# Performance work log

Measured on AMD Instinct MI355X. Metric: run time of the kernel, lower is better.

## Reference

```python
import jax, jax.numpy as jnp
import numpy as np

W = 1022      # window_length (fft_length) -> 512 rfft bins
HOP = 256     # hop_length
F = 64        # frames
ORDER = 5     # butterworth order
WN = 0.5      # normalized cutoff (cutoff = fs/4)

# ---- Butterworth lowpass design (scipy.signal.butter equivalent, numpy only) ----
def _butter_lowpass(order, wn):
    m = np.arange(-order + 1, order, 2)
    p = -np.exp(1j * np.pi * m / (2 * order))        # analog prototype poles
    k = 1.0
    fs = 2.0
    warped = 2 * fs * np.tan(np.pi * wn / fs)        # pre-warp
    p = p * warped                                   # lp2lp
    k = k * warped ** order
    fs2 = 2 * fs                                     # bilinear
    pd = (fs2 + p) / (fs2 - p)
    zd = -np.ones(order)
    kd = k * np.real(1.0 / np.prod(fs2 - p))
    b = np.real(kd * np.poly(zd))
    a = np.real(np.poly(pd))
    return b / a[0], a / a[0]

_B_NP, _A_NP = _butter_lowpass(ORDER, WN)

def _lfilter_zi(b, a):
    n = max(len(a), len(b))
    A = np.zeros((n - 1, n - 1))
    A[0, :] = -a[1:]
    A[1:, :-1] = np.eye(n - 2)
    A = A.T
    Bv = b[1:] - a[1:] * b[0]
    return np.linalg.solve(np.eye(n - 1) - A, Bv)

_ZI_NP = _lfilter_zi(_B_NP, _A_NP)
PADLEN = 3 * max(len(_A_NP), len(_B_NP))  # scipy filtfilt default = 18

B_COEF = jnp.asarray(_B_NP, jnp.float32)
A_COEF = jnp.asarray(_A_NP, jnp.float32)
ZI = jnp.asarray(_ZI_NP, jnp.float32)

# ---- windows (tf.signal defaults: periodic Hann; inverse_stft_window_fn) ----
def _hann(n):
    return 0.5 - 0.5 * np.cos(2.0 * np.pi * np.arange(n) / n)

_FW = _hann(W)
_overlaps = -(-W // HOP)
_den = np.pad(_FW ** 2, (0, _overlaps * HOP - W))
_den = _den.reshape(_overlaps, HOP).sum(0)
_den = np.tile(_den, _overlaps)[:W]
SYN_WIN = jnp.asarray(_FW / _den, jnp.float32)   # synthesis window
FWD_WIN = jnp.asarray(_FW, jnp.float32)          # analysis window

_IDX = np.arange(F)[:, None] * HOP + np.arange(W)[None, :]  # [F, W]
T = HOP * (F - 1) + W  # 17150


def _lfilter(x, zi):
    # direct-form II transposed, batched over axis 0; x: [B,T], zi: [B,n]
    b0, b1, a1 = B_COEF[0], B_COEF[1:], A_COEF[1:]
    def step(z, xt):
        y = b0 * xt + z[:, 0]
        zs = jnp.concatenate([z[:, 1:], jnp.zeros_like(z[:, :1])], axis=1)
        z = zs + xt[:, None] * b1[None, :] - y[:, None] * a1[None, :]
        return z, y
    _, ys = jax.lax.scan(step, zi, x.T)
    return ys.T


def _filtfilt(x):
    # scipy.signal.filtfilt with padtype='odd', padlen=PADLEN
    left = 2.0 * x[:, :1] - x[:, PADLEN:0:-1]
    right = 2.0 * x[:, -1:] - x[:, -2:-PADLEN - 2:-1]
    xe = jnp.concatenate([left, x, right], axis=1)
    y = _lfilter(xe, ZI[None, :] * xe[:, :1])
    y = y[:, ::-1]
    y = _lfilter(y, ZI[None, :] * y[:, :1])
    y = y[:, ::-1]
    return y[:, PADLEN:-PADLEN]


def setup_inputs() -> dict:
    key = jax.random.key(0)
    x = jax.random.normal(key, (64, 512, F, 2), dtype=jnp.float32)
    return {"x": x}


def reference(x):
    bsz = x.shape[0]
    stfts = jax.lax.complex(x[..., 0], x[..., 1])          # [B,512,F]
    frames = jnp.transpose(stfts, (0, 2, 1))               # [B,F,512]
    # inverse STFT: irfft -> synthesis window -> overlap-add
    sig_frames = jnp.fft.irfft(frames, n=W, axis=-1) * SYN_WIN  # [B,F,W]
    signals = jnp.zeros((bsz, T), jnp.float32).at[:, _IDX.reshape(-1)].add(
        sig_frames.reshape(bsz, -1))                       # [B,T]
    filt = _filtfilt(signals)                              # [B,T]
    # forward STFT
    fr = filt[:, _IDX] * FWD_WIN                           # [B,F,W]
    S = jnp.fft.rfft(fr, n=W, axis=-1)                     # [B,F,512]
    S = jnp.transpose(S, (0, 2, 1))                        # [B,512,F]
    return jnp.stack([jnp.real(S), jnp.imag(S)], axis=-1)
```

## Files before the change

### kernel.cpp

```cpp
#include <hip/hip_runtime.h>
#include <cmath>
#include <complex>
#include <algorithm>

#define NW      1022
#define NB      64
#define TLEN    17150
#define PADL    18
#define LXLEN   17186
#define NFRAMES 4096
#define GK      1024
#define BS      4288
#define SPAN    4480

typedef __attribute__((ext_vector_type(8))) short short8;
typedef __attribute__((ext_vector_type(4))) float floatx4;

struct IirCoef {
  float b0,b1,b2,b3,b4,b5;
  float a1,a2,a3,a4,a5;
  float zi0,zi1,zi2,zi3,zi4;
};

static __device__ __forceinline__ ushort f2bf(float f) {
  uint32_t u = __builtin_bit_cast(uint32_t, f);
  uint32_t r = (u + 0x7FFFu + ((u >> 16) & 1u)) >> 16;
  return (ushort)r;
}
static __device__ __forceinline__ float bf2f(ushort u) {
  return __builtin_bit_cast(float, (uint32_t)u << 16);
}

static __device__ __forceinline__ float phase_mod(int k, int t) {
  const float TPN = 6.2831853071795864769f / 1022.f;
  float kt = (float)(k * t);
  float q = floorf(kt * (1.0f / 1022.0f));
  float r = kt - q * 1022.0f;
  if (r < 0.f) r += 1022.f;
  if (r >= 1022.f) r -= 1022.f;
  return r * TPN;
}

__global__ __launch_bounds__(256) void prep(const float* __restrict__ x,
                                            ushort* __restrict__ BT1,
                                            ushort* __restrict__ BT2,
                                            ushort* __restrict__ A1) {
  __shared__ float tile[32][129];
  const float TPN = 6.2831853071795864769f / 1022.f;
  int bid = blockIdx.x;
  if (bid < 4096) {
    int idx = bid * 256 + threadIdx.x;
    int t = idx >> 10, kk = idx & 1023;
    int k = kk & 511;
    float val = 0.f;
    if (t < NW) {
      float fw = 0.5f - 0.5f * __cosf((float)t * TPN);
      float den = 0.f;
      int tm = t & 255;
      #pragma unroll
      for (int j = 0; j < 4; ++j) {
        int u = tm + (j << 8);
        if (u < NW) { float w = 0.5f - 0.5f * __cosf((float)u * TPN); den += w * w; }
      }
      float syn = fw / den;
      float arg = phase_mod(k, t);
      float scale = (k == 0 || k == 511) ? 1.f : 2.f;
      if (kk < 512) val = __cosf(arg) * scale * (1.f / 1022.f) * syn;
      else          val = (k == 0 || k == 511) ? 0.f
                          : -__sinf(arg) * scale * (1.f / 1022.f) * syn;
    }
    BT1[idx] = f2bf(val);
  } else if (bid < 8192) {
    int idx = (bid - 4096) * 256 + threadIdx.x;
    int kk = idx >> 10, t = idx & 1023;
    int k = kk & 511;
    float val = 0.f;
    if (t < NW) {
      float fw = 0.5f - 0.5f * __cosf((float)t * TPN);
      float arg = phase_mod(k, t);
      val = (kk < 512) ? fw * __cosf(arg) : -fw * __sinf(arg);
    }
    BT2[idx] = f2bf(val);
  } else {
    int tb = bid - 8192;
    int b  = tb >> 4;
    int k0 = (tb & 15) << 5;
    int tid = threadIdx.x;
    #pragma unroll
    for (int e = 0; e < 16; ++e) {
      int lin = tid + e * 256;
      int i = lin >> 7, c = lin & 127;
      tile[i][c] = x[(b * 512 + k0 + i) * 128 + c];
    }
    __syncthreads();
    #pragma unroll
    for (int e = 0; e < 16; ++e) {
      int lin = tid + e * 256;
      int c = lin >> 5, i = lin & 31;
      int f = c >> 1, ri = c & 1;
      A1[(b * 64 + f) * 1024 + ri * 512 + k0 + i] = f2bf(tile[i][c]);
    }
  }
}

#define GLOAD16(gsrc, ldst) \
  __builtin_amdgcn_global_load_lds( \
      (const __attribute__((address_space(1))) void*)(gsrc), \
      (__attribute__((address_space(3))) void*)(ldst), 16, 0, 0)

#define WAIT_VMCNT6()  __builtin_amdgcn_s_waitcnt(0xF76)
#define WAIT_VMCNT0()  __builtin_amdgcn_s_waitcnt(0xF70)

static __device__ __forceinline__ void gemm_compute64(
    const ushort* as, const ushort* bs, int arow, int brow, int g, int rx,
    floatx4 (&acc)[2][4]) {
  #pragma unroll
  for (int ks = 0; ks < 2; ++ks) {
    short8 af[2], bfr[4];
    const int chunk = ((ks << 2) + g) ^ rx;
    #pragma unroll
    for (int fm = 0; fm < 2; ++fm)
      af[fm] = *(const short8*)(as + (arow + fm * 16) * 64 + chunk * 8);
    #pragma unroll
    for (int fn = 0; fn < 4; ++fn)
      bfr[fn] = *(const short8*)(bs + (brow + fn * 16) * 64 + chunk * 8);
    #pragma unroll
    for (int fm = 0; fm < 2; ++fm)
      #pragma unroll
      for (int fn = 0; fn < 4; ++fn)
        acc[fm][fn] = __builtin_amdgcn_mfma_f32_16x16x32_bf16(
            af[fm], bfr[fn], acc[fm][fn], 0, 0, 0);
  }
}

__global__ __launch_bounds__(256, 3) void gemm1(
    const ushort* __restrict__ A, const ushort* __restrict__ Bt,
    ushort* __restrict__ Fr) {
  __shared__ __align__(16) ushort As[2][64 * 64];
  __shared__ __align__(16) ushort Bs[2][128 * 64];
  const int tid = threadIdx.x;
  const int wid = tid >> 6, lane = tid & 63;
  const int m0 = blockIdx.y * 64, n0 = blockIdx.x * 128;
  const int warp_m = wid >> 1, warp_n = wid & 1;

  floatx4 acc[2][4];
  #pragma unroll
  for (int i = 0; i < 2; ++i)
    #pragma unroll
    for (int j = 0; j < 4; ++j) acc[i][j] = (floatx4){0.f, 0.f, 0.f, 0.f};

  const int lr = lane >> 3, lc = lane & 7;
  const int swz = lc ^ lr;
  const ushort* aBase = A  + (size_t)(m0 + wid * 8 + lr) * GK + swz * 8;
  const ushort* bBase = Bt + (size_t)(n0 + wid * 8 + lr) * GK + swz * 8;

  const int lane15 = lane & 15;
  const int g = lane >> 4;
  const int rx = lane & 7;
  const int arow = warp_m * 32 + lane15;
  const int brow = warp_n * 64 + lane15;

#define STAGE_G1(buf, kk0) do { \
    _Pragma("unroll") \
    for (int p = 0; p < 2; ++p) \
      GLOAD16(aBase + (size_t)(p * 32) * GK + (kk0), &As[buf][(p * 32 + wid * 8) * 64]); \
    _Pragma("unroll") \
    for (int p = 0; p < 4; ++p) \
      GLOAD16(bBase + (size_t)(p * 32) * GK + (kk0), &Bs[buf][(p * 32 + wid * 8) * 64]); \
    } while (0)

  STAGE_G1(0, 0);
  for (int t = 0; t < 15; ++t) {
    STAGE_G1((t + 1) & 1, (t + 1) * 64);
    WAIT_VMCNT6();
    __builtin_amdgcn_s_barrier();
    __builtin_amdgcn_sched_barrier(0);
    gemm_compute64(&As[t & 1][0], &Bs[t & 1][0], arow, brow, g, rx, acc);
    __builtin_amdgcn_sched_barrier(0);
    __builtin_amdgcn_s_barrier();
  }
  WAIT_VMCNT0();
  __builtin_amdgcn_s_barrier();
  gemm_compute64(&As[1][0], &Bs[1][0], arow, brow, g, rx, acc);

  #pragma unroll
  for (int fm = 0; fm < 2; ++fm)
    #pragma unroll
    for (int fn = 0; fn < 4; ++fn)
      #pragma unroll
      for (int i = 0; i < 4; ++i) {
        int gm = m0 + warp_m * 32 + fm * 16 + g * 4 + i;
        int gn = n0 + warp_n * 64 + fn * 16 + lane15;
        Fr[(size_t)gm * 1024 + gn] = f2bf(acc[fm][fn][i]);
      }
#undef STAGE_G1
}

__global__ __launch_bounds__(256, 3) void gemm2(
    const ushort* __restrict__ Ftb, const ushort* __restrict__ Bt,
    float* __restrict__ out) {
  __shared__ __align__(16) ushort smem[2 * 64 * 64 + 2 * 128 * 64];
  ushort (*As)[64 * 64] = (ushort(*)[64 * 64])smem;
  ushort (*Bs)[128 * 64] = (ushort(*)[128 * 64])(smem + 2 * 64 * 64);
  float* CT = (float*)smem;
  const int tid = threadIdx.x;
  const int wid = tid >> 6, lane = tid & 63;
  const int by = blockIdx.y, bx = blockIdx.x;
  const int warp_m = wid >> 1, warp_n = wid & 1;

  floatx4 acc[2][4];
  #pragma unroll
  for (int i = 0; i < 2; ++i)
    #pragma unroll
    for (int j = 0; j < 4; ++j) acc[i][j] = (floatx4){0.f, 0.f, 0.f, 0.f};

  const int lr = lane >> 3, lc = lane & 7;
  const int swz = lc ^ lr;

  const ushort* aBase = Ftb + (size_t)by * TLEN + (wid * 8 + lr) * 256 + swz * 8;
  const ushort* bB0 = Bt + (size_t)(bx * 64 + wid * 8 + lr) * GK + swz * 8;

  const int lane15 = lane & 15;
  const int g = lane >> 4;
  const int rx = lane & 7;
  const int arow = warp_m * 32 + lane15;
  const int brow = warp_n * 64 + lane15;

#define STAGE_G2(buf, kk0) do { \
    _Pragma("unroll") \
    for (int p = 0; p < 2; ++p) \
      GLOAD16(aBase + (size_t)(p * 32) * 256 + (kk0), &As[buf][(p * 32 + wid * 8) * 64]); \
    _Pragma("unroll") \
    for (int p = 0; p < 4; ++p) { \
      size_t boff = (size_t)((p & 1) * 32 + (p >> 1) * 512) * GK; \
      GLOAD16(bB0 + boff + (kk0), &Bs[buf][(((p >> 1) * 64 + (p & 1) * 32) + wid * 8) * 64]); \
    } } while (0)

  STAGE_G2(0, 0);
  for (int t = 0; t < 15; ++t) {
    STAGE_G2((t + 1) & 1, (t + 1) * 64);
    WAIT_VMCNT6();
    __builtin_amdgcn_s_barrier();
    __builtin_amdgcn_sched_barrier(0);
    gemm_compute64(&As[t & 1][0], &Bs[t & 1][0], arow, brow, g, rx, acc);
    __builtin_amdgcn_sched_barrier(0);
    __builtin_amdgcn_s_barrier();
  }
  WAIT_VMCNT0();
  __builtin_amdgcn_s_barrier();
  gemm_compute64(&As[1][0], &Bs[1][0], arow, brow, g, rx, acc);

  __syncthreads();
  #pragma unroll
  for (int fm = 0; fm < 2; ++fm)
    #pragma unroll
    for (int fn = 0; fn < 4; ++fn)
      #pragma unroll
      for (int i = 0; i < 4; ++i) {
        int s    = warp_n * 64 + fn * 16 + lane15;
        int fcol = warp_m * 32 + fm * 16 + g * 4 + i;
        CT[s * 65 + fcol] = acc[fm][fn][i];
      }
  __syncthreads();
  #pragma unroll
  for (int e = 0; e < 8; ++e) {
    int it = tid + e * 256;
    int r = it >> 5, q = it & 31;
    float4 v;
    v.x = CT[r * 65 + 2 * q];
    v.y = CT[(64 + r) * 65 + 2 * q];
    v.z = CT[r * 65 + 2 * q + 1];
    v.w = CT[(64 + r) * 65 + 2 * q + 1];
    *(float4*)&out[((size_t)(by * 512 + bx * 64 + r)) * 128 + q * 4] = v;
  }
#undef STAGE_G2
}

#define SWZ(r) ((r) ^ (((r) >> 6) & 31))

static __device__ __forceinline__ float oa_sample(const ushort* __restrict__ frb,
                                                  int tau) {
  int fhi = tau >> 8;
  int flo = fhi - 3; if (flo < 0) flo = 0;
  if (fhi > 63) fhi = 63;
  float sum = 0.f;
  for (int f = flo; f <= fhi; ++f) {
    int off = tau - (f << 8);
    if (off < NW) sum += bf2f(frb[(size_t)f * 1024 + off]);
  }
  return sum;
}

#define IIR_STEP(x, y)                                   \
  float y = fmaf(cf.b0, (x), z0);                        \
  z0 = fmaf(-cf.a1, y, fmaf(cf.b1, (x), z1));            \
  z1 = fmaf(-cf.a2, y, fmaf(cf.b2, (x), z2));            \
  z2 = fmaf(-cf.a3, y, fmaf(cf.b3, (x), z3));            \
  z3 = fmaf(-cf.a4, y, fmaf(cf.b4, (x), z4));            \
  z4 = fmaf(-cf.a5, y, cf.b5 * (x));

__global__ __launch_bounds__(256) void oa_iir(const ushort* __restrict__ Fr,
                                              ushort* __restrict__ Ftb,
                                              IirCoef cf) {
  __shared__ float bufX[SPAN];
  __shared__ float bufY[SPAN];
  const int blk = blockIdx.x;
  const int b = blk >> 2, sp = blk & 3;
  const int lo = sp * BS;
  const int hi = (lo + BS < TLEN) ? lo + BS : TLEN;
  const int F0 = (sp == 0) ? 0 : lo + PADL;
  int F1 = hi + PADL + 128; if (F1 > LXLEN) F1 = LXLEN;
  const int XB = (sp == 0) ? 0 : F0 - 64;
  const int xspan = F1 - XB;
  const ushort* frb = Fr + (size_t)(b * 64) * 1024;

  for (int rel = threadIdx.x; rel < xspan; rel += 256) {
    int p = XB + rel;
    float v;
    if (p < PADL)
      v = 2.f * oa_sample(frb, 0) - oa_sample(frb, PADL - p);
    else if (p < PADL + TLEN)
      v = oa_sample(frb, p - PADL);
    else {
      int j = p - (PADL + TLEN);
      v = 2.f * oa_sample(frb, TLEN - 1) - oa_sample(frb, TLEN - 2 - j);
    }
    bufX[SWZ(rel)] = v;
  }
  __syncthreads();

  {
    int nch = (F1 - F0 + 63) >> 6;
    int c = threadIdx.x;
    if (c < nch) {
      int os = F0 + (c << 6);
      int oe = os + 64; if (oe > F1) oe = F1;
      float z0, z1, z2, z3, z4;
      int i;
      if (sp == 0 && c == 0) {
        float x0 = bufX[SWZ(0)];
        z0 = cf.zi0 * x0; z1 = cf.zi1 * x0; z2 = cf.zi2 * x0;
        z3 = cf.zi3 * x0; z4 = cf.zi4 * x0;
        i = 0;
      } else {
        z0 = z1 = z2 = z3 = z4 = 0.f;
        i = os - 64;
        #pragma unroll 4
        for (; i < os; ++i) { float x = bufX[SWZ(i - XB)]; IIR_STEP(x, y); (void)y; }
      }
      #pragma unroll 4
      for (; i < oe; ++i) {
        float x = bufX[SWZ(i - XB)];
        IIR_STEP(x, y);
        bufY[SWZ(i - XB)] = y;
      }
    }
  }
  __syncthreads();

  {
    const int R0 = TLEN + PADL - hi;
    const int R1 = LXLEN - lo - PADL;
    int k_lo = R0 >> 6, k_hi = (R1 - 1) >> 6;
    int k = k_lo + threadIdx.x;
    if (k <= k_hi) {
      int rs = k << 6;
      int re = rs + 64; if (re > R1) re = R1;
      float z0, z1, z2, z3, z4;
      int i;
      if (k == 0) {
        float x0 = bufY[SWZ(LXLEN - 1 - XB)];
        z0 = cf.zi0 * x0; z1 = cf.zi1 * x0; z2 = cf.zi2 * x0;
        z3 = cf.zi3 * x0; z4 = cf.zi4 * x0;
        i = 0;
      } else {
        z0 = z1 = z2 = z3 = z4 = 0.f;
        i = rs - 64;
        #pragma unroll 4
        for (; i < rs; ++i) { float x = bufY[SWZ(LXLEN - 1 - i - XB)]; IIR_STEP(x, y); (void)y; }
      }
      #pragma unroll 4
      for (; i < re; ++i) {
        float x = bufY[SWZ(LXLEN - 1 - i - XB)];
        IIR_STEP(x, y);
        if (i >= R0) bufX[SWZ(LXLEN - 1 - i - XB)] = y;
      }
    }
  }
  __syncthreads();

  for (int t = lo + threadIdx.x; t < hi; t += 256)
    Ftb[(size_t)b * TLEN + t] = f2bf(bufX[SWZ(t + PADL - XB)]);
  if (b == NB - 1 && sp == 3)
    for (int t = threadIdx.x; t < 1024; t += 256)
      Ftb[(size_t)NB * TLEN + t] = 0;
}

static void solve5(double M[5][5], double v[5], double outv[5]) {
  for (int col = 0; col < 5; ++col) {
    int piv = col;
    for (int r = col + 1; r < 5; ++r)
      if (std::fabs(M[r][col]) > std::fabs(M[piv][col])) piv = r;
    if (piv != col) {
      for (int c = 0; c < 5; ++c) std::swap(M[col][c], M[piv][c]);
      std::swap(v[col], v[piv]);
    }
    double d = M[col][col];
    for (int r = col + 1; r < 5; ++r) {
      double f = M[r][col] / d;
      for (int c = col; c < 5; ++c) M[r][c] -= f * M[col][c];
      v[r] -= f * v[col];
    }
  }
  for (int r = 4; r >= 0; --r) {
    double s = v[r];
    for (int c = r + 1; c < 5; ++c) s -= M[r][c] * outv[c];
    outv[r] = s / M[r][r];
  }
}

static IirCoef make_coef() {
  const double PI = 3.14159265358979323846;
  std::complex<double> p[5];
  for (int i = 0; i < 5; ++i) {
    double m = -4.0 + 2.0 * i;
    p[i] = -std::exp(std::complex<double>(0.0, PI * m / 10.0));
  }
  double fs = 2.0;
  double warped = 2.0 * fs * std::tan(PI * 0.5 / fs);
  for (int i = 0; i < 5; ++i) p[i] *= warped;
  double kgain = std::pow(warped, 5.0);
  double fs2 = 2.0 * fs;
  std::complex<double> pd[5], prod(1.0, 0.0);
  for (int i = 0; i < 5; ++i) {
    pd[i] = (fs2 + p[i]) / (fs2 - p[i]);
    prod *= (fs2 - p[i]);
  }
  double kd = kgain * std::real(1.0 / prod);
  double b[6] = {kd, 5 * kd, 10 * kd, 10 * kd, 5 * kd, kd};
  std::complex<double> c[6] = {{1,0},{0,0},{0,0},{0,0},{0,0},{0,0}};
  for (int i = 0; i < 5; ++i)
    for (int j = i + 1; j >= 1; --j)
      c[j] -= pd[i] * c[j - 1];
  double a[6]; for (int i = 0; i < 6; ++i) a[i] = c[i].real();
  double M[5][5], v[5];
  for (int r = 0; r < 5; ++r)
    for (int cc = 0; cc < 5; ++cc) {
      double Af = 0.0;
      if (cc == 0) Af = -a[r + 1];
      if (cc == r + 1) Af = 1.0;
      M[r][cc] = (r == cc ? 1.0 : 0.0) - Af;
    }
  for (int r = 0; r < 5; ++r) v[r] = b[r + 1] - a[r + 1] * b[0];
  double zi[5];
  solve5(M, v, zi);
  IirCoef cf;
  cf.b0 = (float)b[0]; cf.b1 = (float)b[1]; cf.b2 = (float)b[2];
  cf.b3 = (float)b[3]; cf.b4 = (float)b[4]; cf.b5 = (float)b[5];
  cf.a1 = (float)a[1]; cf.a2 = (float)a[2]; cf.a3 = (float)a[3];
  cf.a4 = (float)a[4]; cf.a5 = (float)a[5];
  cf.zi0 = (float)zi[0]; cf.zi1 = (float)zi[1]; cf.zi2 = (float)zi[2];
  cf.zi3 = (float)zi[3]; cf.zi4 = (float)zi[4];
  return cf;
}

extern "C" void kernel_launch(void* const* d_in, const int* in_sizes, int n_in,
                              void* d_out, int out_size, void* d_ws, size_t ws_size,
                              hipStream_t stream) {
  const float* x = (const float*)d_in[0];
  float* out = (float*)d_out;

  ushort* BT1 = (ushort*)d_ws;
  ushort* BT2 = BT1 + 1024 * 1024;
  ushort* A1  = BT2 + 1024 * 1024;
  ushort* Ftb = A1 + (size_t)NFRAMES * 1024;
  ushort* Fr  = Ftb + (size_t)NB * TLEN + 1024;
  size_t need = (size_t)((char*)(Fr + (size_t)NFRAMES * 1024) - (char*)d_ws);
  if (ws_size < need) return;

  IirCoef cf = make_coef();

  prep<<<9216, 256, 0, stream>>>(x, BT1, BT2, A1);
  gemm1<<<dim3(8, 64), 256, 0, stream>>>(A1, BT1, Fr);
  oa_iir<<<NB * 4, 256, 0, stream>>>(Fr, Ftb, cf);
  gemm2<<<dim3(8, 64), 256, 0, stream>>>(Ftb, BT2, out);
}
```

Before: 81.75 us.

## Split IIR into 8 spans, vectorize twiddle prep, move BT2 build into gemm1

The IIR/overlap-add kernel now splits each batch row into 8 spans instead of 4, doubling block count from 256 to 512 for better CU occupancy, at the cost of more warm-up recomputation at span boundaries. The BT1 twiddle generation writes 4 bf16 values per thread with a vector store. BT2 generation moves out of prep into extra blocks of gemm1 so it overlaps with the first GEMM. gemm1 also remaps block indices so neighbouring tiles land on the same XCD for L2 locality.

```diff
diff --git a/kernel.cpp b/kernel.cpp
--- a/kernel.cpp
+++ b/kernel.cpp
@@ -10,10 +10,12 @@
 #define LXLEN   17186
 #define NFRAMES 4096
 #define GK      1024
-#define BS      4288
-#define SPAN    4480
+#define NSPLIT  8
+#define BS      2144
+#define SPAN    2336
 
 typedef __attribute__((ext_vector_type(8))) short short8;
+typedef __attribute__((ext_vector_type(4))) short short4v;
 typedef __attribute__((ext_vector_type(4))) float floatx4;
 
 struct IirCoef {
@@ -43,16 +45,14 @@
 
 __global__ __launch_bounds__(256) void prep(const float* __restrict__ x,
                                             ushort* __restrict__ BT1,
-                                            ushort* __restrict__ BT2,
                                             ushort* __restrict__ A1) {
   __shared__ float tile[32][129];
   const float TPN = 6.2831853071795864769f / 1022.f;
   int bid = blockIdx.x;
-  if (bid < 4096) {
-    int idx = bid * 256 + threadIdx.x;
-    int t = idx >> 10, kk = idx & 1023;
-    int k = kk & 511;
-    float val = 0.f;
+  if (bid < 1024) {
+    int idx4 = (bid * 256 + threadIdx.x) * 4;
+    int t = idx4 >> 10, kk0 = idx4 & 1023;
+    short4v v = (short4v){0, 0, 0, 0};
     if (t < NW) {
       float fw = 0.5f - 0.5f * __cosf((float)t * TPN);
       float den = 0.f;
@@ -63,26 +63,21 @@
         if (u < NW) { float w = 0.5f - 0.5f * __cosf((float)u * TPN); den += w * w; }
       }
       float syn = fw / den;
-      float arg = phase_mod(k, t);
-      float scale = (k == 0 || k == 511) ? 1.f : 2.f;
-      if (kk < 512) val = __cosf(arg) * scale * (1.f / 1022.f) * syn;
-      else          val = (k == 0 || k == 511) ? 0.f
-                          : -__sinf(arg) * scale * (1.f / 1022.f) * syn;
-    }
-    BT1[idx] = f2bf(val);
-  } else if (bid < 8192) {
-    int idx = (bid - 4096) * 256 + threadIdx.x;
-    int kk = idx >> 10, t = idx & 1023;
-    int k = kk & 511;
-    float val = 0.f;
-    if (t < NW) {
-      float fw = 0.5f - 0.5f * __cosf((float)t * TPN);
-      float arg = phase_mod(k, t);
-      val = (kk < 512) ? fw * __cosf(arg) : -fw * __sinf(arg);
-    }
-    BT2[idx] = f2bf(val);
+      #pragma unroll
+      for (int e = 0; e < 4; ++e) {
+        int kk = kk0 + e, k = kk & 511;
+        float arg = phase_mod(k, t);
+        float scale = (k == 0 || k == 511) ? 1.f : 2.f;
+        float val;
+        if (kk < 512) val = __cosf(arg) * scale * (1.f / 1022.f) * syn;
+        else          val = (k == 0 || k == 511) ? 0.f
+                            : -__sinf(arg) * scale * (1.f / 1022.f) * syn;
+        v[e] = (short)f2bf(val);
+      }
+    }
+    *(short4v*)&BT1[idx4] = v;
   } else {
-    int tb = bid - 8192;
+    int tb = bid - 1024;
     int b  = tb >> 4;
     int k0 = (tb & 15) << 5;
     int tid = threadIdx.x;
@@ -135,19 +130,46 @@
 
 __global__ __launch_bounds__(256, 3) void gemm1(
     const ushort* __restrict__ A, const ushort* __restrict__ Bt,
-    ushort* __restrict__ Fr) {
+    ushort* __restrict__ Fr, ushort* __restrict__ BT2) {
   __shared__ __align__(16) ushort As[2][64 * 64];
   __shared__ __align__(16) ushort Bs[2][128 * 64];
+  const float TPN = 6.2831853071795864769f / 1022.f;
+
+  if (blockIdx.y >= 64) {
+    int bid = (blockIdx.y - 64) * 8 + blockIdx.x;
+    int idx4 = (bid * 256 + threadIdx.x) * 4;
+    int kk = idx4 >> 10, t0 = idx4 & 1023;
+    int k = kk & 511;
+    short4v v = (short4v){0, 0, 0, 0};
+    #pragma unroll
+    for (int e = 0; e < 4; ++e) {
+      int t = t0 + e;
+      if (t < NW) {
+        float fw = 0.5f - 0.5f * __cosf((float)t * TPN);
+        float arg = phase_mod(k, t);
+        float val = (kk < 512) ? fw * __cosf(arg) : -fw * __sinf(arg);
+        v[e] = (short)f2bf(val);
+      }
+    }
+    *(short4v*)&BT2[idx4] = v;
+    return;
+  }
+
+  const int L = blockIdx.x + 8 * blockIdx.y;
+  const int xcd = L & 7, j = L >> 3;
+  const int by_n = xcd * 8 + (j & 7);
+  const int bx_n = j >> 3;
+
   const int tid = threadIdx.x;
   const int wid = tid >> 6, lane = tid & 63;
-  const int m0 = blockIdx.y * 64, n0 = blockIdx.x * 128;
+  const int m0 = by_n * 64, n0 = bx_n * 128;
   const int warp_m = wid >> 1, warp_n = wid & 1;
 
   floatx4 acc[2][4];
   #pragma unroll
   for (int i = 0; i < 2; ++i)
     #pragma unroll
-    for (int j = 0; j < 4; ++j) acc[i][j] = (floatx4){0.f, 0.f, 0.f, 0.f};
+    for (int jj = 0; jj < 4; ++jj) acc[i][jj] = (floatx4){0.f, 0.f, 0.f, 0.f};
 
   const int lr = lane >> 3, lc = lane & 7;
   const int swz = lc ^ lr;
@@ -305,7 +327,7 @@
   __shared__ float bufX[SPAN];
   __shared__ float bufY[SPAN];
   const int blk = blockIdx.x;
-  const int b = blk >> 2, sp = blk & 3;
+  const int b = blk >> 3, sp = blk & 7;
   const int lo = sp * BS;
   const int hi = (lo + BS < TLEN) ? lo + BS : TLEN;
   const int F0 = (sp == 0) ? 0 : lo + PADL;
@@ -391,7 +413,7 @@
 
   for (int t = lo + threadIdx.x; t < hi; t += 256)
     Ftb[(size_t)b * TLEN + t] = f2bf(bufX[SWZ(t + PADL - XB)]);
-  if (b == NB - 1 && sp == 3)
+  if (b == NB - 1 && sp == NSPLIT - 1)
     for (int t = threadIdx.x; t < 1024; t += 256)
       Ftb[(size_t)NB * TLEN + t] = 0;
 }
@@ -480,8 +502,8 @@
 
   IirCoef cf = make_coef();
 
-  prep<<<9216, 256, 0, stream>>>(x, BT1, BT2, A1);
-  gemm1<<<dim3(8, 64), 256, 0, stream>>>(A1, BT1, Fr);
-  oa_iir<<<NB * 4, 256, 0, stream>>>(Fr, Ftb, cf);
+  prep<<<2048, 256, 0, stream>>>(x, BT1, A1);
+  gemm1<<<dim3(8, 192), 256, 0, stream>>>(A1, BT1, Fr, BT2);
+  oa_iir<<<NB * NSPLIT, 256, 0, stream>>>(Fr, Ftb, cf);
   gemm2<<<dim3(8, 64), 256, 0, stream>>>(Ftb, BT2, out);
 }
```

After: 68.22 us. -16.5%, faster.
